# Kernel optimization log

Hardware: AMD Instinct MI355X
Metric: run time of the kernel (lower is better)

The kernel has to match this reference:

```python
import jax, jax.numpy as jnp
import numpy as np

B, IN_FEATURES, OUT_FEATURES, N_BASIS = 65536, 128, 16, 16
WEIGHT_MAGNITUDE = 1.0


def chebyshev_basis(x, n):
    # x: [B, IN] in [-1, 1] -> T_k(x) stacked: [B, IN, n]
    Ts = [jnp.ones_like(x), x]
    for _ in range(n - 2):
        Ts.append(2.0 * x * Ts[-1] - Ts[-2])
    return jnp.stack(Ts[:n], axis=-1)


def setup_inputs() -> dict:
    key = jax.random.key(0)
    k1, k2 = jax.random.split(key)
    # inputs assumed normalized to [-1, 1] (polynomial basis domain)
    x = jax.random.uniform(k1, (B, IN_FEATURES), jnp.float32, -1.0, 1.0)
    wm = WEIGHT_MAGNITUDE / IN_FEATURES
    w = jax.random.uniform(k2, (OUT_FEATURES, IN_FEATURES, N_BASIS), jnp.float32, -wm, wm)
    return {"x": x, "w": w}


def reference(x, w):
    # basis expansion [B, IN, N] contracted against w [OUT, IN, N] -> [B, OUT]
    basis = chebyshev_basis(x, w.shape[-1])
    return jnp.einsum('bin,oin->bo', basis, w)
```

## Files before the change

kernel.cpp:

```cpp
#include <hip/hip_runtime.h>
#include <hip/hip_bf16.h>

typedef _Float16 f16x8 __attribute__((ext_vector_type(8)));
typedef __fp16  fp16x2 __attribute__((ext_vector_type(2)));
typedef float f32x4 __attribute__((ext_vector_type(4)));

#define N_ROWS 65536
#define IN_F 128
#define OUT_F 16
#define NB 16


__global__ void prep_w_kernel(const float* __restrict__ w, _Float16* __restrict__ wf) {
    int q = blockIdx.x * 256 + threadIdx.x;
    int j = q & 7;
    int l = (q >> 3) & 63;
    int ks = q >> 9;
    int half = ks & 1;
    int p = ks >> 1;
    int o = l & 15;
    int g = l >> 4;
    int f = 4 * p + g;
    int n = 8 * half + j;
    wf[q] = (_Float16)w[(o * IN_F + f) * NB + n];
}

__device__ __forceinline__ void cheb_frags(float xv, f16x8& ae, f16x8& ao) {
    float x2 = xv + xv;
    float t2  = __builtin_fmaf(x2, xv,  -1.0f);
    float t3  = __builtin_fmaf(x2, t2,  -xv);
    float t4  = __builtin_fmaf(x2, t3,  -t2);
    float t5  = __builtin_fmaf(x2, t4,  -t3);
    float t6  = __builtin_fmaf(x2, t5,  -t4);
    float t7  = __builtin_fmaf(x2, t6,  -t5);
    float t8  = __builtin_fmaf(x2, t7,  -t6);
    float t9  = __builtin_fmaf(x2, t8,  -t7);
    float t10 = __builtin_fmaf(x2, t9,  -t8);
    float t11 = __builtin_fmaf(x2, t10, -t9);
    float t12 = __builtin_fmaf(x2, t11, -t10);
    float t13 = __builtin_fmaf(x2, t12, -t11);
    float t14 = __builtin_fmaf(x2, t13, -t12);
    float t15 = __builtin_fmaf(x2, t14, -t13);
    union { f16x8 v; fp16x2 h[4]; } e, od;
    e.h[0]  = __builtin_amdgcn_cvt_pkrtz(1.0f, xv);
    e.h[1]  = __builtin_amdgcn_cvt_pkrtz(t2,  t3);
    e.h[2]  = __builtin_amdgcn_cvt_pkrtz(t4,  t5);
    e.h[3]  = __builtin_amdgcn_cvt_pkrtz(t6,  t7);
    od.h[0] = __builtin_amdgcn_cvt_pkrtz(t8,  t9);
    od.h[1] = __builtin_amdgcn_cvt_pkrtz(t10, t11);
    od.h[2] = __builtin_amdgcn_cvt_pkrtz(t12, t13);
    od.h[3] = __builtin_amdgcn_cvt_pkrtz(t14, t15);
    ae = e.v;
    ao = od.v;
}

__global__ __launch_bounds__(256) void cheb_main(const float* __restrict__ x,
                                                 const _Float16* __restrict__ wf,
                                                 float* __restrict__ out) {
    __shared__ float xs[128 * 128];
    const int tid = threadIdx.x;
    const long row0 = (long)blockIdx.x * 128;

    const float4* xg = (const float4*)(x + row0 * IN_F);
    #pragma unroll
    for (int it = 0; it < 16; ++it) {
        int idx = it * 256 + tid;
        int r = idx >> 5;
        int c4 = (idx & 31) << 2;
        float4 v = xg[idx];
        *(float4*)&xs[r * 128 + (c4 ^ ((r & 7) << 2))] = v;
    }
    __syncthreads();

    const int l  = tid & 63;
    const int wv = tid >> 6;
    const int g  = l >> 4;
    const int o  = l & 15;
    const int lm = l & 15;
    const int sw = l & 7;

    const int r0 = wv * 32 + lm;
    const int r1 = r0 + 16;

    f32x4 acc0 = {0.f, 0.f, 0.f, 0.f};
    f32x4 acc1 = {0.f, 0.f, 0.f, 0.f};

    const f16x8* wfv = (const f16x8*)wf;

    #pragma unroll 2
    for (int p = 0; p < 32; ++p) {
        f16x8 b0 = wfv[(2 * p) * 64 + l];
        f16x8 b1 = wfv[(2 * p) * 64 + 64 + l];
        int col = ((p ^ sw) << 2) | g;
        float x0 = xs[r0 * 128 + col];
        float x1 = xs[r1 * 128 + col];
        f16x8 a0e, a0o, a1e, a1o;
        cheb_frags(x0, a0e, a0o);
        cheb_frags(x1, a1e, a1o);
        acc0 = __builtin_amdgcn_mfma_f32_16x16x32_f16(a0e, b0, acc0, 0, 0, 0);
        acc0 = __builtin_amdgcn_mfma_f32_16x16x32_f16(a0o, b1, acc0, 0, 0, 0);
        acc1 = __builtin_amdgcn_mfma_f32_16x16x32_f16(a1e, b0, acc1, 0, 0, 0);
        acc1 = __builtin_amdgcn_mfma_f32_16x16x32_f16(a1o, b1, acc1, 0, 0, 0);
    }

    float* op = out + (row0 + wv * 32 + 4 * g) * OUT_F + o;
    #pragma unroll
    for (int rr = 0; rr < 4; ++rr) {
        op[rr * OUT_F] = acc0[rr];
        op[(16 + rr) * OUT_F] = acc1[rr];
    }
}

extern "C" void kernel_launch(void* const* d_in, const int* in_sizes, int n_in,
                              void* d_out, int out_size, void* d_ws, size_t ws_size,
                              hipStream_t stream) {
    const float* x = (const float*)d_in[0];
    const float* w = (const float*)d_in[1];
    float* out = (float*)d_out;
    _Float16* wf = (_Float16*)d_ws;

    prep_w_kernel<<<128, 256, 0, stream>>>(w, wf);
    cheb_main<<<512, 256, 0, stream>>>(x, wf, out);
}
```

Baseline: 19.70 us.

## Split the K dimension across two blocks and combine partial results with atomics

The main kernel now splits the 128 input features into two halves handled by separate blocks. This doubles the grid to 1024 blocks and halves the shared-memory tile so more blocks fit per CU. Partial outputs are accumulated with float atomicAdd into an output that a new memset clears first. The weight prep kernel now reads w coalesced and scatters the writes instead. The trade-off is an extra memset launch, atomic traffic on the output, and a summation order that is no longer deterministic.

```diff
diff --git a/kernel.cpp b/kernel.cpp
--- a/kernel.cpp
+++ b/kernel.cpp
@@ -5,24 +5,19 @@
 typedef __fp16  fp16x2 __attribute__((ext_vector_type(2)));
 typedef float f32x4 __attribute__((ext_vector_type(4)));
 
-#define N_ROWS 65536
 #define IN_F 128
 #define OUT_F 16
 #define NB 16
 
-
 __global__ void prep_w_kernel(const float* __restrict__ w, _Float16* __restrict__ wf) {
     int q = blockIdx.x * 256 + threadIdx.x;
-    int j = q & 7;
-    int l = (q >> 3) & 63;
-    int ks = q >> 9;
-    int half = ks & 1;
-    int p = ks >> 1;
-    int o = l & 15;
-    int g = l >> 4;
-    int f = 4 * p + g;
-    int n = 8 * half + j;
-    wf[q] = (_Float16)w[(o * IN_F + f) * NB + n];
+    int n = q & 15;
+    int f = (q >> 4) & 127;
+    int o = q >> 11;
+    int p = f >> 2, g = f & 3, h = n >> 3, j = n & 7;
+    int ks = 2 * p + h;
+    int l = g * 16 + o;
+    wf[(ks * 64 + l) * 8 + j] = (_Float16)w[q];
 }
 
 __device__ __forceinline__ void cheb_frags(float xv, f16x8& ae, f16x8& ao) {
@@ -57,18 +52,20 @@
 __global__ __launch_bounds__(256) void cheb_main(const float* __restrict__ x,
                                                  const _Float16* __restrict__ wf,
                                                  float* __restrict__ out) {
-    __shared__ float xs[128 * 128];
+    __shared__ float xs[128 * 64];
     const int tid = threadIdx.x;
-    const long row0 = (long)blockIdx.x * 128;
+    const int bid = blockIdx.x;
+    const int kh = bid & 1;
+    const long row0 = (long)(bid >> 1) * 128;
 
     const float4* xg = (const float4*)(x + row0 * IN_F);
     #pragma unroll
-    for (int it = 0; it < 16; ++it) {
+    for (int it = 0; it < 8; ++it) {
         int idx = it * 256 + tid;
-        int r = idx >> 5;
-        int c4 = (idx & 31) << 2;
-        float4 v = xg[idx];
-        *(float4*)&xs[r * 128 + (c4 ^ ((r & 7) << 2))] = v;
+        int r = idx >> 4;
+        int c = idx & 15;
+        float4 v = xg[r * 32 + kh * 16 + c];
+        *(float4*)&xs[r * 64 + ((c ^ (r & 7)) << 2)] = v;
     }
     __syncthreads();
 
@@ -87,13 +84,14 @@
 
     const f16x8* wfv = (const f16x8*)wf;
 
-    #pragma unroll 2
-    for (int p = 0; p < 32; ++p) {
-        f16x8 b0 = wfv[(2 * p) * 64 + l];
-        f16x8 b1 = wfv[(2 * p) * 64 + 64 + l];
-        int col = ((p ^ sw) << 2) | g;
-        float x0 = xs[r0 * 128 + col];
-        float x1 = xs[r1 * 128 + col];
+    #pragma unroll 4
+    for (int p = 0; p < 16; ++p) {
+        int pg = kh * 16 + p;
+        f16x8 b0 = wfv[(2 * pg) * 64 + l];
+        f16x8 b1 = wfv[(2 * pg) * 64 + 64 + l];
+        int col = (((p ^ sw) & 15) << 2) | g;
+        float x0 = xs[r0 * 64 + col];
+        float x1 = xs[r1 * 64 + col];
         f16x8 a0e, a0o, a1e, a1o;
         cheb_frags(x0, a0e, a0o);
         cheb_frags(x1, a1e, a1o);
@@ -106,8 +104,8 @@
     float* op = out + (row0 + wv * 32 + 4 * g) * OUT_F + o;
     #pragma unroll
     for (int rr = 0; rr < 4; ++rr) {
-        op[rr * OUT_F] = acc0[rr];
-        op[(16 + rr) * OUT_F] = acc1[rr];
+        atomicAdd(&op[rr * OUT_F], acc0[rr]);
+        atomicAdd(&op[(16 + rr) * OUT_F], acc1[rr]);
     }
 }
 
@@ -120,5 +118,6 @@
     _Float16* wf = (_Float16*)d_ws;
 
     prep_w_kernel<<<128, 256, 0, stream>>>(w, wf);
-    cheb_main<<<512, 256, 0, stream>>>(x, wf, out);
+    hipMemsetAsync(out, 0, (size_t)out_size * sizeof(float), stream);
+    cheb_main<<<1024, 256, 0, stream>>>(x, wf, out);
 }
```

Result: slower. 24.40 us (+23.9%).

## Load x directly from global as float4 per lane, drop LDS staging

Applied to the files above, without the earlier changes.

Removes the shared-memory staging of the x tile and its barrier; each lane now reads float4 chunks of x straight from global memory. The loop is reordered so four consecutive features come from one vector load, and the weight prep kernel's feature-to-k-step mapping is remapped to match, with coalesced reads of w. This frees 64KB of LDS per block, which can raise occupancy and removes the sync. In exchange the global loads are less coalesced: each lane reads 16 bytes from a different row.

```diff
diff --git a/kernel.cpp b/kernel.cpp
--- a/kernel.cpp
+++ b/kernel.cpp
@@ -5,24 +5,20 @@
 typedef __fp16  fp16x2 __attribute__((ext_vector_type(2)));
 typedef float f32x4 __attribute__((ext_vector_type(4)));
 
-#define N_ROWS 65536
 #define IN_F 128
 #define OUT_F 16
 #define NB 16
 
-
 __global__ void prep_w_kernel(const float* __restrict__ w, _Float16* __restrict__ wf) {
-    int q = blockIdx.x * 256 + threadIdx.x;
-    int j = q & 7;
-    int l = (q >> 3) & 63;
-    int ks = q >> 9;
-    int half = ks & 1;
-    int p = ks >> 1;
-    int o = l & 15;
-    int g = l >> 4;
-    int f = 4 * p + g;
-    int n = 8 * half + j;
-    wf[q] = (_Float16)w[(o * IN_F + f) * NB + n];
+    int qi = blockIdx.x * 256 + threadIdx.x;
+    int n = qi & 15;
+    int f = (qi >> 4) & 127;
+    int o = qi >> 11;
+    int P = f >> 4, rem = f & 15, g = rem >> 2, q = rem & 3;
+    int h = n >> 3, j = n & 7;
+    int ks = 8 * P + 2 * q + h;
+    int l = g * 16 + o;
+    wf[(ks * 64 + l) * 8 + j] = (_Float16)w[qi];
 }
 
 __device__ __forceinline__ void cheb_frags(float xv, f16x8& ae, f16x8& ao) {
@@ -57,50 +53,41 @@
 __global__ __launch_bounds__(256) void cheb_main(const float* __restrict__ x,
                                                  const _Float16* __restrict__ wf,
                                                  float* __restrict__ out) {
-    __shared__ float xs[128 * 128];
     const int tid = threadIdx.x;
     const long row0 = (long)blockIdx.x * 128;
-
-    const float4* xg = (const float4*)(x + row0 * IN_F);
-    #pragma unroll
-    for (int it = 0; it < 16; ++it) {
-        int idx = it * 256 + tid;
-        int r = idx >> 5;
-        int c4 = (idx & 31) << 2;
-        float4 v = xg[idx];
-        *(float4*)&xs[r * 128 + (c4 ^ ((r & 7) << 2))] = v;
-    }
-    __syncthreads();
 
     const int l  = tid & 63;
     const int wv = tid >> 6;
     const int g  = l >> 4;
     const int o  = l & 15;
     const int lm = l & 15;
-    const int sw = l & 7;
 
-    const int r0 = wv * 32 + lm;
-    const int r1 = r0 + 16;
+    const long r0 = row0 + wv * 32 + lm;
+    const long r1 = r0 + 16;
+
+    const f32x4* x4 = (const f32x4*)x;
+    const f16x8* wfv = (const f16x8*)wf;
 
     f32x4 acc0 = {0.f, 0.f, 0.f, 0.f};
     f32x4 acc1 = {0.f, 0.f, 0.f, 0.f};
 
-    const f16x8* wfv = (const f16x8*)wf;
-
-    #pragma unroll 2
-    for (int p = 0; p < 32; ++p) {
-        f16x8 b0 = wfv[(2 * p) * 64 + l];
-        f16x8 b1 = wfv[(2 * p) * 64 + 64 + l];
-        int col = ((p ^ sw) << 2) | g;
-        float x0 = xs[r0 * 128 + col];
-        float x1 = xs[r1 * 128 + col];
-        f16x8 a0e, a0o, a1e, a1o;
-        cheb_frags(x0, a0e, a0o);
-        cheb_frags(x1, a1e, a1o);
-        acc0 = __builtin_amdgcn_mfma_f32_16x16x32_f16(a0e, b0, acc0, 0, 0, 0);
-        acc0 = __builtin_amdgcn_mfma_f32_16x16x32_f16(a0o, b1, acc0, 0, 0, 0);
-        acc1 = __builtin_amdgcn_mfma_f32_16x16x32_f16(a1e, b0, acc1, 0, 0, 0);
-        acc1 = __builtin_amdgcn_mfma_f32_16x16x32_f16(a1o, b1, acc1, 0, 0, 0);
+    #pragma unroll
+    for (int P = 0; P < 8; ++P) {
+        f32x4 xv0 = x4[r0 * 32 + P * 4 + g];
+        f32x4 xv1 = x4[r1 * 32 + P * 4 + g];
+        #pragma unroll
+        for (int q = 0; q < 4; ++q) {
+            int ks = 8 * P + 2 * q;
+            f16x8 b0 = wfv[ks * 64 + l];
+            f16x8 b1 = wfv[ks * 64 + 64 + l];
+            f16x8 a0e, a0o, a1e, a1o;
+            cheb_frags(xv0[q], a0e, a0o);
+            cheb_frags(xv1[q], a1e, a1o);
+            acc0 = __builtin_amdgcn_mfma_f32_16x16x32_f16(a0e, b0, acc0, 0, 0, 0);
+            acc0 = __builtin_amdgcn_mfma_f32_16x16x32_f16(a0o, b1, acc0, 0, 0, 0);
+            acc1 = __builtin_amdgcn_mfma_f32_16x16x32_f16(a1e, b0, acc1, 0, 0, 0);
+            acc1 = __builtin_amdgcn_mfma_f32_16x16x32_f16(a1o, b1, acc1, 0, 0, 0);
+        }
     }
 
     float* op = out + (row0 + wv * 32 + 4 * g) * OUT_F + o;
```

Result: no change. 19.70 us (-0.0%).
